# Kernel tuning notes

Measured on AMD Instinct MI355X. Metric: run time of the kernel, lower is better.

Reference implementation:

```python
import jax, jax.numpy as jnp
import numpy as np

IN_DIM = 64

def setup_inputs() -> dict:
    key = jax.random.key(0)
    ks = jax.random.split(key, 9)
    B, C, H, W = 4, IN_DIM, 256, 256
    scale = 1.0 / np.sqrt(3 * C)  # conv fan-in init scale
    return {
        'rgb': jax.random.normal(ks[0], (B, C, H, W), dtype=jnp.float32),
        'hsv': jax.random.normal(ks[1], (B, C, H, W), dtype=jnp.float32),
        'lab': jax.random.normal(ks[2], (B, C, H, W), dtype=jnp.float32),
        'Wq': jax.random.normal(ks[3], (C, 3 * C), dtype=jnp.float32) * scale,
        'bq': jax.random.normal(ks[4], (C,), dtype=jnp.float32) * scale,
        'Wk': jax.random.normal(ks[5], (C, 3 * C), dtype=jnp.float32) * scale,
        'bk': jax.random.normal(ks[6], (C,), dtype=jnp.float32) * scale,
        'Wv': jax.random.normal(ks[7], (C, 3 * C), dtype=jnp.float32) * scale,
        'bv': jax.random.normal(ks[8], (C,), dtype=jnp.float32) * scale,
    }

def _proj(x, W, b):
    # 1x1 conv: [B,3C,H,W] x [C,3C] -> [B,C,H,W]
    return jnp.einsum('oc,bchw->bohw', W, x) + b[None, :, None, None]

def reference(rgb, hsv, lab, Wq, bq, Wk, bk, Wv, bv):
    B, C, H, W = rgb.shape
    combined = jnp.concatenate([rgb, hsv, lab], axis=1)  # [B,3C,H,W]
    q = _proj(combined, Wq, bq).reshape(B, C, H * W)     # [B,C,N]
    k = _proj(combined, Wk, bk).reshape(B, C, H * W)     # [B,C,N]
    v = _proj(combined, Wv, bv).reshape(B, C, H * W)     # [B,C,N]
    energy = jnp.einsum('bcn,bdn->bcd', q, k) * (C ** -0.5)  # [B,C,C]
    attention = jax.nn.softmax(energy, axis=-1)
    out = jnp.einsum('bcd,bdn->bcn', attention, v)           # [B,C,N]
    return out.reshape(B, C, H, W)
```

## Files before the change

### kernel.cpp

```cpp
#include <hip/hip_runtime.h>
#include <cstddef>


#define NPIX 65536

typedef _Float16 half4_t __attribute__((ext_vector_type(4)));
typedef _Float16 half8_t __attribute__((ext_vector_type(8)));
typedef float f32x4_t __attribute__((ext_vector_type(4)));

constexpr int TRI_I[78] = {
  0,0,0,0,0,0,0,0,0,0,0,0,
  1,1,1,1,1,1,1,1,1,1,1,
  2,2,2,2,2,2,2,2,2,2,
  3,3,3,3,3,3,3,3,3,
  4,4,4,4,4,4,4,4,
  5,5,5,5,5,5,5,
  6,6,6,6,6,6,
  7,7,7,7,7,
  8,8,8,8,
  9,9,9,
  10,10,
  11};
constexpr int TRI_J[78] = {
  0,1,2,3,4,5,6,7,8,9,10,11,
  1,2,3,4,5,6,7,8,9,10,11,
  2,3,4,5,6,7,8,9,10,11,
  3,4,5,6,7,8,9,10,11,
  4,5,6,7,8,9,10,11,
  5,6,7,8,9,10,11,
  6,7,8,9,10,11,
  7,8,9,10,11,
  8,9,10,11,
  9,10,11,
  10,11,
  11};

#define PSZ 20160

__global__ void k0_zero(float* __restrict__ p, int n) {
  int i = blockIdx.x * 256 + threadIdx.x;
  if (i < n) p[i] = 0.0f;
}

template <int BASE, int CNT>
__device__ __forceinline__ void mfma_run(const _Float16* __restrict__ buf,
                                         f32x4_t* __restrict__ acc, int l15, int g) {
  half8_t fA;
#pragma unroll
  for (int tt = 0; tt < CNT; ++tt) {
    const int t = BASE + tt;
    if (tt == 0 || TRI_I[t] != TRI_I[t - 1]) {
      int rA = TRI_I[t] * 16 + l15;
      fA = *(const half8_t*)(buf + rA * 32 + ((g ^ ((rA >> 1) & 3)) << 3));
    }
    int rB = TRI_J[t] * 16 + l15;
    half8_t fB = *(const half8_t*)(buf + rB * 32 + ((g ^ ((rB >> 1) & 3)) << 3));
    acc[tt] = __builtin_amdgcn_mfma_f32_16x16x32_f16(fA, fB, acc[tt], 0, 0, 0);
  }
}

template <int BASE, int CNT>
__device__ __forceinline__ void flush_part(const f32x4_t* __restrict__ acc,
                                           float* __restrict__ pb, int lane) {
#pragma unroll
  for (int tt = 0; tt < CNT; ++tt)
    *(f32x4_t*)(pb + (BASE + tt) * 256 + lane * 4) = acc[tt];
}

template <int BASE, int CNT>
__device__ __forceinline__ void flush_atomic(const f32x4_t* __restrict__ acc,
                                             float* __restrict__ Gb, int lane) {
#pragma unroll
  for (int tt = 0; tt < CNT; ++tt) {
    const int t = BASE + tt;
#pragma unroll
    for (int r = 0; r < 4; ++r) {
      int gr = TRI_I[t] * 16 + ((lane >> 4) << 2) + r;
      int gc = TRI_J[t] * 16 + (lane & 15);
      atomicAdd(Gb + gr * 192 + gc, acc[tt][r]);
    }
  }
}

__global__ __launch_bounds__(512) void k1_gram(
    const float* __restrict__ rgb, const float* __restrict__ hsv, const float* __restrict__ lab,
    float* __restrict__ G, float* __restrict__ S, float* __restrict__ part, int mode) {
  __shared__ alignas(16) _Float16 lds[12288];
  float* slds = (float*)lds;

  const int t = threadIdx.x;
  const int lane = t & 63;
  const int w = t >> 6;
  const int b = blockIdx.y;
  const int bx = blockIdx.x;
  const int n0 = bx * 512;

  const int gq = t & 7;
  const int r6 = t >> 3;
  const float* gp0 = rgb + (size_t)(b * 64 + r6) * NPIX + n0 + 4 * gq;
  const float* gp1 = hsv + (size_t)(b * 64 + r6) * NPIX + n0 + 4 * gq;
  const float* gp2 = lab + (size_t)(b * 64 + r6) * NPIX + n0 + 4 * gq;
  const int wsw = (((gq >> 1) ^ ((r6 >> 1) & 3)) << 3) + (gq & 1) * 4;
  const int wof0 = (0 * 64 + r6) * 32 + wsw;
  const int wof1 = (1 * 64 + r6) * 32 + wsw;
  const int wof2 = (2 * 64 + r6) * 32 + wsw;

  f32x4_t acc[10];
  const f32x4_t zero4 = {0.0f, 0.0f, 0.0f, 0.0f};
#pragma unroll
  for (int i = 0; i < 10; ++i) acc[i] = zero4;
  float sr0 = 0.f, sr1 = 0.f, sr2 = 0.f;

  float4 P[6];
  auto loadR = [&](int cc) {
#pragma unroll
    for (int ks = 0; ks < 2; ++ks) {
      P[0 * 2 + ks] = *(const float4*)(gp0 + cc * 64 + ks * 32);
      P[1 * 2 + ks] = *(const float4*)(gp1 + cc * 64 + ks * 32);
      P[2 * 2 + ks] = *(const float4*)(gp2 + cc * 64 + ks * 32);
    }
  };
  auto writeL = [&]() {
    half4_t h;
#pragma unroll
    for (int ks = 0; ks < 2; ++ks) {
      float4 p0 = P[0 * 2 + ks], p1 = P[1 * 2 + ks], p2 = P[2 * 2 + ks];
      sr0 += (p0.x + p0.y) + (p0.z + p0.w);
      h.x = (_Float16)p0.x; h.y = (_Float16)p0.y; h.z = (_Float16)p0.z; h.w = (_Float16)p0.w;
      *(half4_t*)(lds + ks * 6144 + wof0) = h;
      sr1 += (p1.x + p1.y) + (p1.z + p1.w);
      h.x = (_Float16)p1.x; h.y = (_Float16)p1.y; h.z = (_Float16)p1.z; h.w = (_Float16)p1.w;
      *(half4_t*)(lds + ks * 6144 + wof1) = h;
      sr2 += (p2.x + p2.y) + (p2.z + p2.w);
      h.x = (_Float16)p2.x; h.y = (_Float16)p2.y; h.z = (_Float16)p2.z; h.w = (_Float16)p2.w;
      *(half4_t*)(lds + ks * 6144 + wof2) = h;
    }
  };

  const int l15 = lane & 15;
  const int g = lane >> 4;

  loadR(0);
  for (int cc = 0; cc < 8; ++cc) {
    writeL();
    __syncthreads();
    if (cc + 1 < 8) loadR(cc + 1);
#pragma unroll
    for (int ks = 0; ks < 2; ++ks) {
      const _Float16* buf = lds + ks * 6144;
      switch (w) {
        case 0: mfma_run<0, 10>(buf, acc, l15, g); break;
        case 1: mfma_run<10, 10>(buf, acc, l15, g); break;
        case 2: mfma_run<20, 10>(buf, acc, l15, g); break;
        case 3: mfma_run<30, 10>(buf, acc, l15, g); break;
        case 4: mfma_run<40, 10>(buf, acc, l15, g); break;
        case 5: mfma_run<50, 10>(buf, acc, l15, g); break;
        case 6: mfma_run<60, 10>(buf, acc, l15, g); break;
        case 7: mfma_run<70, 8>(buf, acc, l15, g); break;
      }
    }
    __syncthreads();
  }

  if (mode) {
    float* pb = part + (size_t)(b * 128 + bx) * PSZ;
    switch (w) {
      case 0: flush_part<0, 10>(acc, pb, lane); break;
      case 1: flush_part<10, 10>(acc, pb, lane); break;
      case 2: flush_part<20, 10>(acc, pb, lane); break;
      case 3: flush_part<30, 10>(acc, pb, lane); break;
      case 4: flush_part<40, 10>(acc, pb, lane); break;
      case 5: flush_part<50, 10>(acc, pb, lane); break;
      case 6: flush_part<60, 10>(acc, pb, lane); break;
      case 7: flush_part<70, 8>(acc, pb, lane); break;
    }
  } else {
    float* Gb = G + b * 36864;
    switch (w) {
      case 0: flush_atomic<0, 10>(acc, Gb, lane); break;
      case 1: flush_atomic<10, 10>(acc, Gb, lane); break;
      case 2: flush_atomic<20, 10>(acc, Gb, lane); break;
      case 3: flush_atomic<30, 10>(acc, Gb, lane); break;
      case 4: flush_atomic<40, 10>(acc, Gb, lane); break;
      case 5: flush_atomic<50, 10>(acc, Gb, lane); break;
      case 6: flush_atomic<60, 10>(acc, Gb, lane); break;
      case 7: flush_atomic<70, 8>(acc, Gb, lane); break;
    }
  }

  __syncthreads();
  slds[(0 * 64 + r6) * 8 + gq] = sr0;
  slds[(1 * 64 + r6) * 8 + gq] = sr1;
  slds[(2 * 64 + r6) * 8 + gq] = sr2;
  __syncthreads();
  if (t < 192) {
    float v = 0.f;
#pragma unroll
    for (int q = 0; q < 8; ++q) v += slds[t * 8 + q];
    if (mode)
      part[(size_t)(b * 128 + bx) * PSZ + 19968 + t] = v;
    else
      atomicAdd(S + b * 192 + t, v);
  }
}

__global__ void k1r_reduce(const float* __restrict__ part, float* __restrict__ G,
                           float* __restrict__ S) {
  int idx = blockIdx.x * 256 + threadIdx.x;
  if (idx >= 4 * PSZ) return;
  int b = idx / PSZ;
  int flat = idx % PSZ;
  const float* base = part + (size_t)b * 128 * PSZ + flat;
  float v0 = 0.f, v1 = 0.f, v2 = 0.f, v3 = 0.f;
#pragma unroll 4
  for (int q = 0; q < 128; q += 4) {
    v0 += base[(size_t)(q + 0) * PSZ];
    v1 += base[(size_t)(q + 1) * PSZ];
    v2 += base[(size_t)(q + 2) * PSZ];
    v3 += base[(size_t)(q + 3) * PSZ];
  }
  float v = (v0 + v1) + (v2 + v3);
  if (flat < 19968) {
    int tt = flat >> 8;
    int r = flat & 255;
    int lane = r >> 2, rg = r & 3;
    int row = TRI_I[tt] * 16 + ((lane >> 4) << 2) + rg;
    int col = TRI_J[tt] * 16 + (lane & 15);
    float* Gb = G + b * 36864;
    Gb[row * 192 + col] = v;
    Gb[col * 192 + row] = v;
  } else {
    S[b * 192 + (flat - 19968)] = v;
  }
}

__global__ void k1m_mirror(float* __restrict__ G) {
  int b = blockIdx.y;
  int idx = blockIdx.x * 256 + threadIdx.x;
  int i = idx / 192, j = idx % 192;
  if ((i >> 4) > (j >> 4)) G[b * 36864 + idx] = G[b * 36864 + j * 192 + i];
}

__global__ __launch_bounds__(256) void k2_small(
    const float* __restrict__ G, const float* __restrict__ S,
    const float* __restrict__ Wq, const float* __restrict__ bq,
    const float* __restrict__ Wk, const float* __restrict__ bk,
    const float* __restrict__ Wv, const float* __restrict__ bv,
    _Float16* __restrict__ Mh, float* __restrict__ c0w) {
  const int b = blockIdx.y;
  const int cbase = blockIdx.x * 8;
  const int t = threadIdx.x;
  __shared__ float T1[192 * 9];
  __shared__ float el[64 * 8];
  __shared__ float sq[8];
  __shared__ float sk[64];
  const float* Gb = G + b * 36864;
  const float* Sb = S + b * 192;

  if (t < 8) {
    float a = 0.f;
    const float* wq = Wq + (cbase + t) * 192;
    for (int i = 0; i < 192; ++i) a = fmaf(wq[i], Sb[i], a);
    sq[t] = a;
  } else if (t < 72) {
    int d = t - 8;
    float a = 0.f;
    const float* wk = Wk + d * 192;
    for (int j = 0; j < 192; ++j) a = fmaf(wk[j], Sb[j], a);
    sk[d] = a;
  }
  for (int e = t; e < 1536; e += 256) {
    int j = e % 192, cp = e / 192;
    const float* wq = Wq + (cbase + cp) * 192;
    float a = 0.f;
    for (int i = 0; i < 192; ++i) a = fmaf(wq[i], Gb[i * 192 + j], a);
    T1[j * 9 + cp] = a;
  }
  __syncthreads();
  for (int e = t; e < 512; e += 256) {
    int cp = e & 7, d = e >> 3;
    const float* wk = Wk + d * 192;
    float a = 0.f;
    for (int j = 0; j < 192; ++j) a = fmaf(T1[j * 9 + cp], wk[j], a);
    float bqc = bq[cbase + cp], bkd = bk[d];
    a += bqc * sk[d] + bkd * sq[cp] + 65536.0f * bqc * bkd;
    el[d * 8 + cp] = a * 0.125f;
  }
  __syncthreads();
  if (t < 8) {
    float mx = -3.0e38f;
    for (int d = 0; d < 64; ++d) mx = fmaxf(mx, el[d * 8 + t]);
    float sum = 0.f;
    for (int d = 0; d < 64; ++d) {
      float pv = expf(el[d * 8 + t] - mx);
      el[d * 8 + t] = pv;
      sum += pv;
    }
    float inv = 1.0f / sum;
    for (int d = 0; d < 64; ++d) el[d * 8 + t] *= inv;
  }
  __syncthreads();
  for (int e = t; e < 1536; e += 256) {
    int i = e % 192, cp = e / 192;
    int c = cbase + cp;
    float a = 0.f;
    for (int d = 0; d < 64; ++d) a = fmaf(el[d * 8 + cp], Wv[d * 192 + i], a);
    Mh[(size_t)b * 12288 + c * 192 + (i ^ ((c & 7) << 3))] = (_Float16)a;
  }
  if (t < 8) {
    float a = 0.f;
    for (int d = 0; d < 64; ++d) a = fmaf(el[d * 8 + t], bv[d], a);
    c0w[b * 64 + cbase + t] = a;
  }
}

__global__ __launch_bounds__(256, 3) void k3_out(
    const float* __restrict__ rgb, const float* __restrict__ hsv, const float* __restrict__ lab,
    const _Float16* __restrict__ Mh, const float* __restrict__ c0w, float* __restrict__ out) {
  __shared__ alignas(16) _Float16 lds_m[12288];
  __shared__ alignas(16) _Float16 lds_x[8192];
  __shared__ float c0l[64];
  const int t = threadIdx.x;
  const int lane = t & 63;
  const int w = t >> 6;
  const int b = blockIdx.y;
  const int nblk = blockIdx.x * 256;

  {
    const float4* msrc = (const float4*)(Mh + (size_t)b * 12288);
    float4* mdst = (float4*)lds_m;
#pragma unroll
    for (int k = 0; k < 6; ++k) mdst[t + 256 * k] = msrc[t + 256 * k];
    if (t < 64) c0l[t] = c0w[b * 64 + t];
  }

  const int xi = t & 31;
  const int ng = t >> 5;
  const float* srcs[3] = {rgb, hsv, lab};

  f32x4_t acc[4][4];
  const f32x4_t zero4 = {0.0f, 0.0f, 0.0f, 0.0f};
#pragma unroll
  for (int i = 0; i < 4; ++i)
#pragma unroll
    for (int j = 0; j < 4; ++j) acc[i][j] = zero4;

  float4 xr[8];
  auto xload = [&](int kc) {
    int ig = kc * 32 + xi;
    const float* p = srcs[ig >> 6] + (size_t)(b * 64 + (ig & 63)) * NPIX + nblk + ng * 32;
#pragma unroll
    for (int f = 0; f < 8; ++f) xr[f] = *(const float4*)(p + f * 4);
  };
  auto xwrite = [&]() {
#pragma unroll
    for (int f = 0; f < 8; ++f) {
      int n = ng * 32 + f * 4;
      lds_x[(n + 0) * 32 + (xi ^ 0)]  = (_Float16)xr[f].x;
      lds_x[(n + 1) * 32 + (xi ^ 8)]  = (_Float16)xr[f].y;
      lds_x[(n + 2) * 32 + (xi ^ 16)] = (_Float16)xr[f].z;
      lds_x[(n + 3) * 32 + (xi ^ 24)] = (_Float16)xr[f].w;
    }
  };

  const int g = lane >> 4;
  const int l15 = lane & 15;

  xload(0);
  for (int kc = 0; kc < 6; ++kc) {
    xwrite();
    __syncthreads();
    if (kc + 1 < 6) xload(kc + 1);
    half8_t fx[4], fm[4];
#pragma unroll
    for (int nt = 0; nt < 4; ++nt) {
      int n = w * 64 + nt * 16 + l15;
      fx[nt] = *(const half8_t*)(lds_x + n * 32 + ((8 * g) ^ ((n & 3) << 3)));
    }
#pragma unroll
    for (int ct = 0; ct < 4; ++ct) {
      int c = ct * 16 + l15;
      fm[ct] = *(const half8_t*)(lds_m + c * 192 + ((kc * 32 + 8 * g) ^ ((c & 7) << 3)));
    }
#pragma unroll
    for (int nt = 0; nt < 4; ++nt)
#pragma unroll
      for (int ct = 0; ct < 4; ++ct)
        acc[nt][ct] = __builtin_amdgcn_mfma_f32_16x16x32_f16(fx[nt], fm[ct], acc[nt][ct], 0, 0, 0);
    __syncthreads();
  }

#pragma unroll
  for (int ct = 0; ct < 4; ++ct) {
    int c = ct * 16 + l15;
    float c0v = c0l[c];
#pragma unroll
    for (int nt = 0; nt < 4; ++nt) {
      int n = nblk + w * 64 + nt * 16 + 4 * g;
      float4 o;
      o.x = acc[nt][ct][0] + c0v;
      o.y = acc[nt][ct][1] + c0v;
      o.z = acc[nt][ct][2] + c0v;
      o.w = acc[nt][ct][3] + c0v;
      *(float4*)(out + (size_t)(b * 64 + c) * NPIX + n) = o;
    }
  }
}

extern "C" void kernel_launch(void* const* d_in, const int* in_sizes, int n_in,
                              void* d_out, int out_size, void* d_ws, size_t ws_size,
                              hipStream_t stream) {
  const float* rgb = (const float*)d_in[0];
  const float* hsv = (const float*)d_in[1];
  const float* lab = (const float*)d_in[2];
  const float* Wq = (const float*)d_in[3];
  const float* bq = (const float*)d_in[4];
  const float* Wk = (const float*)d_in[5];
  const float* bk = (const float*)d_in[6];
  const float* Wv = (const float*)d_in[7];
  const float* bv = (const float*)d_in[8];
  float* out = (float*)d_out;
  float* ws = (float*)d_ws;

  float* G = ws;
  float* S = ws + 147456;
  _Float16* Mh = (_Float16*)(ws + 148224);
  float* c0w = ws + 172800;
  float* part = ws + 173056;
  const size_t need1 = (size_t)(173056 + 4 * 128 * PSZ) * 4;
  const int mode = ws_size >= need1 ? 1 : 0;

  if (!mode)
    k0_zero<<<dim3(579), dim3(256), 0, stream>>>(ws, 148224);

  k1_gram<<<dim3(128, 4), dim3(512), 0, stream>>>(rgb, hsv, lab, G, S, part, mode);
  if (mode)
    k1r_reduce<<<dim3(315), dim3(256), 0, stream>>>(part, G, S);
  else
    k1m_mirror<<<dim3(144, 4), dim3(256), 0, stream>>>(G);
  k2_small<<<dim3(8, 4), dim3(256), 0, stream>>>(G, S, Wq, bq, Wk, bk, Wv, bv, Mh, c0w);
  k3_out<<<dim3(256, 4), dim3(256), 0, stream>>>(rgb, hsv, lab, Mh, c0w, out);
}
```

Baseline: 150.8 us.

## Double-buffer LDS in gram kernel, halve grid, compute row sums from LDS

```diff
diff --git a/kernel.cpp b/kernel.cpp
--- a/kernel.cpp
+++ b/kernel.cpp
@@ -3,6 +3,7 @@
 
 
 #define NPIX 65536
+#define SUBSTRIDE 6160
 
 typedef _Float16 half4_t __attribute__((ext_vector_type(4)));
 typedef _Float16 half8_t __attribute__((ext_vector_type(8)));
@@ -85,69 +86,64 @@
 __global__ __launch_bounds__(512) void k1_gram(
     const float* __restrict__ rgb, const float* __restrict__ hsv, const float* __restrict__ lab,
     float* __restrict__ G, float* __restrict__ S, float* __restrict__ part, int mode) {
-  __shared__ alignas(16) _Float16 lds[12288];
-  float* slds = (float*)lds;
+  __shared__ alignas(16) _Float16 lds[2][4 * SUBSTRIDE];
 
   const int t = threadIdx.x;
   const int lane = t & 63;
   const int w = t >> 6;
   const int b = blockIdx.y;
   const int bx = blockIdx.x;
-  const int n0 = bx * 512;
-
-  const int gq = t & 7;
-  const int r6 = t >> 3;
-  const float* gp0 = rgb + (size_t)(b * 64 + r6) * NPIX + n0 + 4 * gq;
-  const float* gp1 = hsv + (size_t)(b * 64 + r6) * NPIX + n0 + 4 * gq;
-  const float* gp2 = lab + (size_t)(b * 64 + r6) * NPIX + n0 + 4 * gq;
-  const int wsw = (((gq >> 1) ^ ((r6 >> 1) & 3)) << 3) + (gq & 1) * 4;
-  const int wof0 = (0 * 64 + r6) * 32 + wsw;
-  const int wof1 = (1 * 64 + r6) * 32 + wsw;
-  const int wof2 = (2 * 64 + r6) * 32 + wsw;
+  const int n0 = bx * 1024;
+
+  const int w24 = w * 24;
+  const int lhi = lane >> 5;
+  const int llo = lane & 31;
+  const int ksw = llo >> 3;
+  const int gq = llo & 7;
 
   f32x4_t acc[10];
   const f32x4_t zero4 = {0.0f, 0.0f, 0.0f, 0.0f};
 #pragma unroll
   for (int i = 0; i < 10; ++i) acc[i] = zero4;
-  float sr0 = 0.f, sr1 = 0.f, sr2 = 0.f;
-
-  float4 P[6];
-  auto loadR = [&](int cc) {
-#pragma unroll
-    for (int ks = 0; ks < 2; ++ks) {
-      P[0 * 2 + ks] = *(const float4*)(gp0 + cc * 64 + ks * 32);
-      P[1 * 2 + ks] = *(const float4*)(gp1 + cc * 64 + ks * 32);
-      P[2 * 2 + ks] = *(const float4*)(gp2 + cc * 64 + ks * 32);
+  float srow = 0.0f;
+
+  float4 P[12];
+  auto stage_issue = [&](int h) {
+#pragma unroll
+    for (int m = 0; m < 12; ++m) {
+      int rp = w24 + 2 * m;
+      const float* sp = (rp < 64) ? rgb : (rp < 128) ? hsv : lab;
+      P[m] = *(const float4*)(sp + (size_t)(b * 64 + (rp & 63) + lhi) * NPIX +
+                              n0 + h * 128 + 4 * llo);
     }
   };
-  auto writeL = [&]() {
-    half4_t h;
-#pragma unroll
-    for (int ks = 0; ks < 2; ++ks) {
-      float4 p0 = P[0 * 2 + ks], p1 = P[1 * 2 + ks], p2 = P[2 * 2 + ks];
-      sr0 += (p0.x + p0.y) + (p0.z + p0.w);
-      h.x = (_Float16)p0.x; h.y = (_Float16)p0.y; h.z = (_Float16)p0.z; h.w = (_Float16)p0.w;
-      *(half4_t*)(lds + ks * 6144 + wof0) = h;
-      sr1 += (p1.x + p1.y) + (p1.z + p1.w);
-      h.x = (_Float16)p1.x; h.y = (_Float16)p1.y; h.z = (_Float16)p1.z; h.w = (_Float16)p1.w;
-      *(half4_t*)(lds + ks * 6144 + wof1) = h;
-      sr2 += (p2.x + p2.y) + (p2.z + p2.w);
-      h.x = (_Float16)p2.x; h.y = (_Float16)p2.y; h.z = (_Float16)p2.z; h.w = (_Float16)p2.w;
-      *(half4_t*)(lds + ks * 6144 + wof2) = h;
+  auto stage_write = [&](int h) {
+    _Float16* buf = &lds[h & 1][0];
+#pragma unroll
+    for (int m = 0; m < 12; ++m) {
+      int row = w24 + 2 * m + lhi;
+      int wof = ksw * SUBSTRIDE + row * 32 +
+                (((gq >> 1) ^ ((row >> 1) & 3)) << 3) + (gq & 1) * 4;
+      float4 p = P[m];
+      half4_t hh;
+      hh.x = (_Float16)p.x; hh.y = (_Float16)p.y;
+      hh.z = (_Float16)p.z; hh.w = (_Float16)p.w;
+      *(half4_t*)(buf + wof) = hh;
     }
   };
 
   const int l15 = lane & 15;
   const int g = lane >> 4;
 
-  loadR(0);
-  for (int cc = 0; cc < 8; ++cc) {
-    writeL();
+  stage_issue(0);
+  for (int h = 0; h < 8; ++h) {
+    stage_write(h);
     __syncthreads();
-    if (cc + 1 < 8) loadR(cc + 1);
-#pragma unroll
-    for (int ks = 0; ks < 2; ++ks) {
-      const _Float16* buf = lds + ks * 6144;
+    if (h + 1 < 8) stage_issue(h + 1);
+    const _Float16* bb = &lds[h & 1][0];
+#pragma unroll
+    for (int ks = 0; ks < 4; ++ks) {
+      const _Float16* buf = bb + ks * SUBSTRIDE;
       switch (w) {
         case 0: mfma_run<0, 10>(buf, acc, l15, g); break;
         case 1: mfma_run<10, 10>(buf, acc, l15, g); break;
@@ -159,11 +155,22 @@
         case 7: mfma_run<70, 8>(buf, acc, l15, g); break;
       }
     }
-    __syncthreads();
+    if (t < 192) {
+      float s = 0.f;
+#pragma unroll
+      for (int ks = 0; ks < 4; ++ks)
+#pragma unroll
+        for (int pp = 0; pp < 4; ++pp) {
+          half8_t v = *(const half8_t*)(bb + ks * SUBSTRIDE + t * 32 + pp * 8);
+          s += ((float)v[0] + (float)v[1]) + ((float)v[2] + (float)v[3]) +
+               ((float)v[4] + (float)v[5]) + ((float)v[6] + (float)v[7]);
+        }
+      srow += s;
+    }
   }
 
   if (mode) {
-    float* pb = part + (size_t)(b * 128 + bx) * PSZ;
+    float* pb = part + (size_t)(b * 64 + bx) * PSZ;
     switch (w) {
       case 0: flush_part<0, 10>(acc, pb, lane); break;
       case 1: flush_part<10, 10>(acc, pb, lane); break;
@@ -174,6 +181,7 @@
       case 6: flush_part<60, 10>(acc, pb, lane); break;
       case 7: flush_part<70, 8>(acc, pb, lane); break;
     }
+    if (t < 192) part[(size_t)(b * 64 + bx) * PSZ + 19968 + t] = srow;
   } else {
     float* Gb = G + b * 36864;
     switch (w) {
@@ -186,34 +194,20 @@
       case 6: flush_atomic<60, 10>(acc, Gb, lane); break;
       case 7: flush_atomic<70, 8>(acc, Gb, lane); break;
     }
-  }
-
-  __syncthreads();
-  slds[(0 * 64 + r6) * 8 + gq] = sr0;
-  slds[(1 * 64 + r6) * 8 + gq] = sr1;
-  slds[(2 * 64 + r6) * 8 + gq] = sr2;
-  __syncthreads();
-  if (t < 192) {
-    float v = 0.f;
-#pragma unroll
-    for (int q = 0; q < 8; ++q) v += slds[t * 8 + q];
-    if (mode)
-      part[(size_t)(b * 128 + bx) * PSZ + 19968 + t] = v;
-    else
-      atomicAdd(S + b * 192 + t, v);
+    if (t < 192) atomicAdd(S + b * 192 + t, srow);
   }
 }
 
 __global__ void k1r_reduce(const float* __restrict__ part, float* __restrict__ G,
-                           float* __restrict__ S) {
+                           float* __restrict__ S, int P) {
   int idx = blockIdx.x * 256 + threadIdx.x;
   if (idx >= 4 * PSZ) return;
   int b = idx / PSZ;
   int flat = idx % PSZ;
-  const float* base = part + (size_t)b * 128 * PSZ + flat;
+  const float* base = part + (size_t)b * P * PSZ + flat;
   float v0 = 0.f, v1 = 0.f, v2 = 0.f, v3 = 0.f;
 #pragma unroll 4
-  for (int q = 0; q < 128; q += 4) {
+  for (int q = 0; q < P; q += 4) {
     v0 += base[(size_t)(q + 0) * PSZ];
     v1 += base[(size_t)(q + 1) * PSZ];
     v2 += base[(size_t)(q + 2) * PSZ];
@@ -427,15 +421,15 @@
   _Float16* Mh = (_Float16*)(ws + 148224);
   float* c0w = ws + 172800;
   float* part = ws + 173056;
-  const size_t need1 = (size_t)(173056 + 4 * 128 * PSZ) * 4;
+  const size_t need1 = (size_t)(173056 + 4 * 64 * PSZ) * 4;
   const int mode = ws_size >= need1 ? 1 : 0;
 
   if (!mode)
     k0_zero<<<dim3(579), dim3(256), 0, stream>>>(ws, 148224);
 
-  k1_gram<<<dim3(128, 4), dim3(512), 0, stream>>>(rgb, hsv, lab, G, S, part, mode);
+  k1_gram<<<dim3(64, 4), dim3(512), 0, stream>>>(rgb, hsv, lab, G, S, part, mode);
   if (mode)
-    k1r_reduce<<<dim3(315), dim3(256), 0, stream>>>(part, G, S);
+    k1r_reduce<<<dim3(315), dim3(256), 0, stream>>>(part, G, S, 64);
   else
     k1m_mirror<<<dim3(144, 4), dim3(256), 0, stream>>>(G);
   k2_small<<<dim3(8, 4), dim3(256), 0, stream>>>(G, S, Wq, bq, Wk, bk, Wv, bv, Mh, c0w);
```

Measured after the change: 263.8 us. 1.75x slower.
